# Kernel optimization log

Measured on AMD Instinct MI355X. Metric: run time of the kernel, lower is better.

Reference implementation:

```python
import jax, jax.numpy as jnp
import numpy as np

V, E, H, K, B, T = 50000, 256, 512, 12, 32, 256
START, STOP = 10, 11
NEG = -10000.0
Hd = H // 2


def _lstm(x, h0, c0, Wih, Whh, bih, bhh):
    # x: [T, B, D] -> hidden states [T, B, Hd]; PyTorch gate order i,f,g,o
    def step(carry, xt):
        h, c = carry
        g = xt @ Wih.T + bih + h @ Whh.T + bhh
        i, f, gg, o = jnp.split(g, 4, axis=-1)
        c = jax.nn.sigmoid(f) * c + jax.nn.sigmoid(i) * jnp.tanh(gg)
        h = jax.nn.sigmoid(o) * jnp.tanh(c)
        return (h, c), h
    _, hs = jax.lax.scan(step, (h0, c0), x)
    return hs


def setup_inputs() -> dict:
    key = jax.random.key(0)
    ks = jax.random.split(key, 12)
    inp = {}
    inp["sentence"] = jax.random.randint(ks[0], (B, T), 0, V, dtype=jnp.int32)
    lens = jax.random.randint(ks[1], (B,), 1, T + 1, dtype=jnp.int32)
    inp["seq_lens"] = jnp.sort(lens)[::-1]  # pack_padded requires descending
    emb = jax.random.normal(ks[2], (V, E)) * 0.05
    inp["emb"] = emb.at[0].set(0.0)  # padding_idx=0
    def lw(k):
        a, b, c, d = jax.random.split(k, 4)
        return (jax.random.normal(a, (4 * Hd, E)) * 0.05,
                jax.random.normal(b, (4 * Hd, Hd)) * 0.05,
                jax.random.normal(c, (4 * Hd,)) * 0.05,
                jax.random.normal(d, (4 * Hd,)) * 0.05)
    inp["Wih_f"], inp["Whh_f"], inp["bih_f"], inp["bhh_f"] = lw(ks[3])
    inp["Wih_b"], inp["Whh_b"], inp["bih_b"], inp["bhh_b"] = lw(ks[4])
    inp["h0"] = jax.random.normal(ks[5], (2, B, Hd))  # init_hidden uses randn
    inp["c0"] = jax.random.normal(ks[6], (2, B, Hd))
    inp["W_out"] = jax.random.normal(ks[7], (K, H)) * 0.05
    inp["b_out"] = jax.random.normal(ks[8], (K,)) * 0.05
    trans = jax.random.normal(ks[9], (K, K))
    inp["transitions"] = trans.at[START, :].set(NEG).at[:, STOP].set(NEG)
    return inp


def _features(sentence, seq_lens, emb, Wih_f, Whh_f, bih_f, bhh_f,
              Wih_b, Whh_b, bih_b, bhh_b, h0, c0, W_out, b_out):
    x = emb[sentence]                       # [B,T,E]
    t_idx = jnp.arange(T)
    # forward direction
    hf = _lstm(x.transpose(1, 0, 2), h0[0], c0[0], Wih_f, Whh_f, bih_f, bhh_f)
    hf = hf.transpose(1, 0, 2)              # [B,T,Hd]
    # backward direction: reverse each sequence within its length (packed semantics)
    rev_idx = jnp.where(t_idx[None, :] < seq_lens[:, None],
                        seq_lens[:, None] - 1 - t_idx[None, :], t_idx[None, :])  # [B,T]
    x_rev = jnp.take_along_axis(x, rev_idx[:, :, None], axis=1)
    hb_rev = _lstm(x_rev.transpose(1, 0, 2), h0[1], c0[1], Wih_b, Whh_b, bih_b, bhh_b)
    hb = jnp.take_along_axis(hb_rev.transpose(1, 0, 2), rev_idx[:, :, None], axis=1)
    hcat = jnp.concatenate([hf, hb], axis=-1)  # [B,T,H]
    return hcat @ W_out.T + b_out              # [B,T,K]


def _viterbi(feats, seq_lens, transitions):
    t_idx = jnp.arange(T)
    mask = t_idx[None, :] < seq_lens[:, None]           # [B,T]
    init = jnp.full((B, K), NEG).at[:, START].set(0.0)  # forward_var

    def vstep(fv, inputs):
        feat_t, m_t = inputs                            # [B,K], [B]
        scores = fv[:, None, :] + transitions[None, :, :]   # [B, next, prev]
        bp = jnp.argmax(scores, axis=-1)                # [B,K]
        best = jnp.max(scores, axis=-1) + feat_t
        return jnp.where(m_t[:, None], best, fv), bp

    fv, bps = jax.lax.scan(vstep, init, (feats.transpose(1, 0, 2), mask.T))
    terminal = fv + transitions[STOP][None, :]          # [B,K]
    best_last = jnp.argmax(terminal, axis=-1)           # [B]
    path_scores = jnp.take_along_axis(terminal, best_last[:, None], axis=1)[:, 0]

    def btstep(tag, inputs):
        bp_t, m_t = inputs
        pred_t = jnp.where(m_t, tag, -1)
        prev = jnp.take_along_axis(bp_t, tag[:, None], axis=1)[:, 0]
        return jnp.where(m_t, prev, tag), pred_t

    _, preds_rev = jax.lax.scan(btstep, best_last, (bps[::-1], mask.T[::-1]))
    preds = preds_rev[::-1].transpose(1, 0)             # [B,T], -1 past seq_len
    return path_scores, preds


def reference(sentence, seq_lens, emb, Wih_f, Whh_f, bih_f, bhh_f,
              Wih_b, Whh_b, bih_b, bhh_b, h0, c0, W_out, b_out, transitions):
    feats = _features(sentence, seq_lens, emb, Wih_f, Whh_f, bih_f, bhh_f,
                      Wih_b, Whh_b, bih_b, bhh_b, h0, c0, W_out, b_out)
    scores, preds = _viterbi(feats, seq_lens, transitions)
    return scores, preds
```

## Files before the change

kernel.cpp:

```cpp
#include <hip/hip_runtime.h>
#include <math.h>

#define T_ 256
#define B_ 32
#define E_ 256
#define HD_ 256
#define NG_ 1024
#define K_ 12
#define START_ 10
#define STOP_ 11
#define NEG_ -10000.0f
#define MAGICU 0x40000000u

typedef float f4_t __attribute__((ext_vector_type(4)));

__device__ __forceinline__ float sigf(float x) { return 1.0f / (1.0f + expf(-x)); }

__global__ void tok_gather(const int* __restrict__ sent, const int* __restrict__ lens,
                           int* __restrict__ tokA) {
    int e = blockIdx.x * 256 + threadIdx.x;
    int dir = e >> 13, m = e & 8191, t = m >> 5, b = m & 31;
    int len = lens[b];
    int tt = dir ? (t < len ? len - 1 - t : t) : t;
    tokA[e] = sent[b * T_ + tt];
}

__global__ void whh_tr(const float* __restrict__ Wf, const float* __restrict__ Wb,
                       float* __restrict__ WT) {
    int dir = blockIdx.x >> 8, k = blockIdx.x & 255, u = threadIdx.x;
    const float* W = dir ? Wb : Wf;
    float4 v;
    v.x = W[(0 * HD_ + u) * HD_ + k];
    v.y = W[(1 * HD_ + u) * HD_ + k];
    v.z = W[(2 * HD_ + u) * HD_ + k];
    v.w = W[(3 * HD_ + u) * HD_ + k];
    ((float4*)(WT + ((size_t)dir * 256 + k) * NG_))[u] = v;
}

__global__ void hex_init(float* __restrict__ hex) {
    int i = blockIdx.x * 256 + threadIdx.x;
    float4 m = make_float4(2.0f, 2.0f, 2.0f, 2.0f);
    ((float4*)hex)[i] = m;
}

__global__ __launch_bounds__(256) void in_gemm(
    const float* __restrict__ emb, const int* __restrict__ tokA,
    const float* __restrict__ Wih_f, const float* __restrict__ Wih_b,
    const float* __restrict__ bih_f, const float* __restrict__ bhh_f,
    const float* __restrict__ bih_b, const float* __restrict__ bhh_b,
    float* __restrict__ G) {
    const int dir = blockIdx.z;
    const int n0 = blockIdx.x * 128, m0 = blockIdx.y * 128;
    const float* Wih = dir ? Wih_b : Wih_f;
    const float* bihp = dir ? bih_b : bih_f;
    const float* bhhp = dir ? bhh_b : bhh_f;
    __shared__ float As[8][128];
    __shared__ float Bs[8][128];
    const int tid = threadIdx.x;
    const int rs = tid >> 1, kc = (tid & 1) * 4;
    const int tok = tokA[dir * 8192 + m0 + rs];
    const float* arow = emb + (size_t)tok * E_;
    const int np = n0 + rs;
    const int wrow = ((np & 3) << 8) | (np >> 2);
    const float* brow = Wih + (size_t)wrow * E_;
    const int ty = tid >> 4, tx = tid & 15;

    float acc[8][8];
#pragma unroll
    for (int i = 0; i < 8; ++i)
#pragma unroll
        for (int j = 0; j < 8; ++j) acc[i][j] = 0.f;

    for (int k0 = 0; k0 < E_; k0 += 8) {
        float4 av = *(const float4*)(arow + k0 + kc);
        float4 bv = *(const float4*)(brow + k0 + kc);
        __syncthreads();
        As[kc + 0][rs] = av.x; As[kc + 1][rs] = av.y; As[kc + 2][rs] = av.z; As[kc + 3][rs] = av.w;
        Bs[kc + 0][rs] = bv.x; Bs[kc + 1][rs] = bv.y; Bs[kc + 2][rs] = bv.z; Bs[kc + 3][rs] = bv.w;
        __syncthreads();
#pragma unroll
        for (int k = 0; k < 8; ++k) {
            float4 a0 = *(const float4*)&As[k][ty * 8];
            float4 a1 = *(const float4*)&As[k][ty * 8 + 4];
            float4 b0 = *(const float4*)&Bs[k][tx * 8];
            float4 b1 = *(const float4*)&Bs[k][tx * 8 + 4];
            float af8[8] = {a0.x, a0.y, a0.z, a0.w, a1.x, a1.y, a1.z, a1.w};
            float bf8[8] = {b0.x, b0.y, b0.z, b0.w, b1.x, b1.y, b1.z, b1.w};
#pragma unroll
            for (int i = 0; i < 8; ++i)
#pragma unroll
                for (int j = 0; j < 8; ++j) acc[i][j] += af8[i] * bf8[j];
        }
    }
    float bias[8];
#pragma unroll
    for (int j = 0; j < 8; ++j) {
        int nn = n0 + tx * 8 + j;
        int wr = ((nn & 3) << 8) | (nn >> 2);
        bias[j] = bihp[wr] + bhhp[wr];
    }
#pragma unroll
    for (int i = 0; i < 8; ++i) {
        int m = m0 + ty * 8 + i;
        float* gp = G + ((size_t)dir * 8192 + m) * NG_ + n0 + tx * 8;
        float4 o0 = {acc[i][0] + bias[0], acc[i][1] + bias[1], acc[i][2] + bias[2], acc[i][3] + bias[3]};
        float4 o1 = {acc[i][4] + bias[4], acc[i][5] + bias[5], acc[i][6] + bias[6], acc[i][7] + bias[7]};
        *(float4*)gp = o0;
        *(float4*)(gp + 4) = o1;
    }
}

__global__ __launch_bounds__(512, 1) void lstm_rec8(
    const float* __restrict__ WhhT, const float* __restrict__ G,
    const float* __restrict__ h0, const float* __restrict__ c0,
    const int* __restrict__ lens, float* __restrict__ hex) {
    const int wg = blockIdx.x;
    const int dir = wg >> 5, bt = (wg >> 3) & 3, ut = wg & 7;
    const int tid = threadIdx.x;
    const int wv = tid >> 6, ln = tid & 63;
    const int upair = ln & 15;
    const int kssub = ln >> 4;
    const int ksup = wv >> 1, bh = wv & 1;
    const int ks = ksup * 4 + kssub;
    const int sb = bh * 4 + (ln & 3);
    const int sk = ksup * 64 + (ln >> 2) * 4;
    const int speer = sk >> 5;

    __shared__ float4 hsA4[256];
    __shared__ float4 hsB4[256];
    __shared__ float4 red4[512 * 11];
    __shared__ float4 hT4[64];

    const int Tmax = lens[bt * 8];

    const float4* WT4 = (const float4*)(WhhT + (size_t)dir * 256 * NG_);
    const int gu_e = ut * 32 + upair * 2;
    float4 We[16], Wo[16];
#pragma unroll
    for (int j = 0; j < 16; ++j) {
        We[j] = WT4[(ks * 16 + j) * 256 + gu_e];
        Wo[j] = WT4[(ks * 16 + j) * 256 + gu_e + 1];
    }

    const bool is_act = (ln < 32);
    float c = 0.f;
    float4 gpend = make_float4(0.f, 0.f, 0.f, 0.f);
    const float* Gd = G + (size_t)dir * 8192 * NG_;
    if (is_act) {
        c = c0[(dir * B_ + bt * 8 + wv) * HD_ + ut * 32 + ln];
        gpend = ((const float4*)(Gd + (size_t)(bt * 8 + wv) * NG_))[ut * 32 + ln];
    }

    float* hexg = hex + (size_t)(dir * 4 + bt) * T_ * 2048;
    float4* hsX4 = bh ? hsB4 : hsA4;
    float* hsX = (float*)hsX4;

    f4_t pend;

    for (int t = 0; t < Tmax; ++t) {
        float4 hv;
        if (t == 0) {
            hv = *(const float4*)(h0 + (size_t)(dir * B_ + bt * 8 + sb) * HD_ + sk);
        } else if (speer == ut) {
            hv = hT4[sb * 8 + ((sk & 31) >> 2)];
        } else {
            asm volatile("s_waitcnt vmcnt(0)" ::: "memory");
            hv.x = pend.x; hv.y = pend.y; hv.z = pend.z; hv.w = pend.w;
            if (__float_as_uint(hv.x) == MAGICU || __float_as_uint(hv.y) == MAGICU ||
                __float_as_uint(hv.z) == MAGICU || __float_as_uint(hv.w) == MAGICU) {
                const float* src = hexg + (size_t)(t - 1) * 2048 + sb * 256 + sk;
                int it = 0;
                for (;;) {
                    __builtin_amdgcn_s_sleep(1);
                    float a0 = __hip_atomic_load(src + 0, __ATOMIC_RELAXED, __HIP_MEMORY_SCOPE_AGENT);
                    float a1 = __hip_atomic_load(src + 1, __ATOMIC_RELAXED, __HIP_MEMORY_SCOPE_AGENT);
                    float a2 = __hip_atomic_load(src + 2, __ATOMIC_RELAXED, __HIP_MEMORY_SCOPE_AGENT);
                    float a3 = __hip_atomic_load(src + 3, __ATOMIC_RELAXED, __HIP_MEMORY_SCOPE_AGENT);
                    if (!(__float_as_uint(a0) == MAGICU || __float_as_uint(a1) == MAGICU ||
                          __float_as_uint(a2) == MAGICU || __float_as_uint(a3) == MAGICU)) {
                        hv = make_float4(a0, a1, a2, a3); break;
                    }
                    if (++it > (1 << 22)) break;
                }
            }
        }
        hsX[(sk + 0) * 4 + (ln & 3)] = hv.x;
        hsX[(sk + 1) * 4 + (ln & 3)] = hv.y;
        hsX[(sk + 2) * 4 + (ln & 3)] = hv.z;
        hsX[(sk + 3) * 4 + (ln & 3)] = hv.w;
        asm volatile("s_waitcnt lgkmcnt(0)" ::: "memory");

        float4 ae0 = {0,0,0,0}, ae1 = {0,0,0,0}, ae2 = {0,0,0,0}, ae3 = {0,0,0,0};
        float4 ao0 = {0,0,0,0}, ao1 = {0,0,0,0}, ao2 = {0,0,0,0}, ao3 = {0,0,0,0};
#pragma unroll
        for (int j = 0; j < 16; ++j) {
            float4 h4 = hsX4[ks * 16 + j];
            float4 we = We[j], wo = Wo[j];
            ae0.x += we.x*h4.x; ae0.y += we.y*h4.x; ae0.z += we.z*h4.x; ae0.w += we.w*h4.x;
            ae1.x += we.x*h4.y; ae1.y += we.y*h4.y; ae1.z += we.z*h4.y; ae1.w += we.w*h4.y;
            ae2.x += we.x*h4.z; ae2.y += we.y*h4.z; ae2.z += we.z*h4.z; ae2.w += we.w*h4.z;
            ae3.x += we.x*h4.w; ae3.y += we.y*h4.w; ae3.z += we.z*h4.w; ae3.w += we.w*h4.w;
            ao0.x += wo.x*h4.x; ao0.y += wo.y*h4.x; ao0.z += wo.z*h4.x; ao0.w += wo.w*h4.x;
            ao1.x += wo.x*h4.y; ao1.y += wo.y*h4.y; ao1.z += wo.z*h4.y; ao1.w += wo.w*h4.y;
            ao2.x += wo.x*h4.z; ao2.y += wo.y*h4.z; ao2.z += wo.z*h4.z; ao2.w += wo.w*h4.z;
            ao3.x += wo.x*h4.w; ao3.y += wo.y*h4.w; ao3.z += wo.z*h4.w; ao3.w += wo.w*h4.w;
        }
        {
            float4* r = &red4[((wv * 4 + kssub) * 16 + upair) * 11 + kssub];
            r[0] = ae0; r[1] = ae1; r[2] = ae2; r[3] = ae3;
            r[4] = ao0; r[5] = ao1; r[6] = ao2; r[7] = ao3;
        }
        asm volatile("s_waitcnt lgkmcnt(0)\n\ts_barrier" ::: "memory");

        if (is_act) {
            const int b = wv, u = ln;
            const int bhv = b >> 2, bq = b & 3, up = u >> 1, par = u & 1;
            float si = gpend.x, sf = gpend.y, sg = gpend.z, so = gpend.w;
#pragma unroll
            for (int kq = 0; kq < 4; ++kq)
#pragma unroll
                for (int kr = 0; kr < 4; ++kr) {
                    float4 p = red4[(((kq * 2 + bhv) * 4 + kr) * 16 + up) * 11 + kr + par * 4 + bq];
                    si += p.x; sf += p.y; sg += p.z; so += p.w;
                }
            c = sigf(sf) * c + sigf(si) * tanhf(sg);
            float h = sigf(so) * tanhf(c);
            ((float*)hT4)[b * 32 + u] = h;
            float* dst = hexg + (size_t)t * 2048 + b * 256 + ut * 32 + u;
            asm volatile("global_store_dword %0, %1, off sc0 sc1" :: "v"(dst), "v"(h) : "memory");
            if (t + 1 < Tmax)
                gpend = ((const float4*)(Gd + ((size_t)(t + 1) * B_ + bt * 8 + b) * NG_))[ut * 32 + u];
        }
        if (t + 1 < Tmax && speer != ut) {
            const float* nsrc = hexg + (size_t)t * 2048 + sb * 256 + sk;
            asm volatile("global_load_dwordx4 %0, %1, off sc0 sc1"
                         : "=v"(pend) : "v"(nsrc) : "memory");
        }
        asm volatile("s_waitcnt lgkmcnt(0)\n\ts_barrier" ::: "memory");
    }
}

__global__ void feat_k(const float* __restrict__ hex, const int* __restrict__ lens,
                       const float* __restrict__ Wout, const float* __restrict__ bout,
                       float* __restrict__ feats) {
    int tid = threadIdx.x;
    int pl = tid / 12, k = tid % 12;
    int p = blockIdx.x * 16 + pl;
    int b = p >> 8, t = p & 255;
    int len = lens[b];
    int tr = t < len ? len - 1 - t : t;
    const float4* hf = (const float4*)(hex + ((size_t)(b >> 3) * T_ + t) * 2048 + (b & 7) * 256);
    const float4* hb = (const float4*)(hex + ((size_t)(4 + (b >> 3)) * T_ + tr) * 2048 + (b & 7) * 256);
    const float4* w0 = (const float4*)(Wout + (size_t)k * 512);
    const float4* w1 = (const float4*)(Wout + (size_t)k * 512 + 256);
    float acc = bout[k];
#pragma unroll 4
    for (int j = 0; j < 64; ++j) {
        float4 h4 = hf[j], v4 = w0[j];
        acc += h4.x * v4.x + h4.y * v4.y + h4.z * v4.z + h4.w * v4.w;
    }
#pragma unroll 4
    for (int j = 0; j < 64; ++j) {
        float4 h4 = hb[j], v4 = w1[j];
        acc += h4.x * v4.x + h4.y * v4.y + h4.z * v4.z + h4.w * v4.w;
    }
    feats[(size_t)p * K_ + k] = acc;
}

__global__ __launch_bounds__(512) void viterbi_k(
    const float* __restrict__ feats, const float* __restrict__ trans,
    const int* __restrict__ lens, float* __restrict__ out) {
    __shared__ float fv[2][B_][16];
    __shared__ float tl[K_][16];
    __shared__ unsigned char bp[T_][B_][6];
    __shared__ int best_last[B_];
    int tid = threadIdx.x;
    int b = tid >> 4, lane = tid & 15;
    if (tid < K_ * K_) tl[tid / 12][tid % 12] = trans[tid];
    if (lane < K_) fv[0][b][lane] = (lane == START_) ? 0.f : NEG_;
    __syncthreads();
    int len = lens[b];
    int pp = 0;
    float f_cur = 0.f;
    if (lane < K_) f_cur = feats[(size_t)b * T_ * K_ + lane];
    for (int t = 0; t < T_; ++t) {
        float f_nxt = 0.f;
        if (t + 1 < T_ && lane < K_) f_nxt = feats[((size_t)b * T_ + t + 1) * K_ + lane];
        if (lane < K_) {
            float best = fv[pp][b][0] + tl[lane][0];
            int argp = 0;
#pragma unroll
            for (int p = 1; p < K_; ++p) {
                float v = fv[pp][b][p] + tl[lane][p];
                if (v > best) { best = v; argp = p; }
            }
            float nb = best + f_cur;
            fv[pp ^ 1][b][lane] = (t < len) ? nb : fv[pp][b][lane];
            int other = __shfl_xor(argp, 1);
            if ((lane & 1) == 0) bp[t][b][lane >> 1] = (unsigned char)(argp | (other << 4));
        }
        __syncthreads();
        pp ^= 1;
        f_cur = f_nxt;
    }
    if (lane == 0) {
        float best = fv[pp][b][0] + tl[STOP_][0];
        int bl = 0;
#pragma unroll
        for (int p = 1; p < K_; ++p) {
            float v = fv[pp][b][p] + tl[STOP_][p];
            if (v > best) { best = v; bl = p; }
        }
        out[b] = best;
        best_last[b] = bl;
    }
    __syncthreads();
    if (lane == 0) {
        int tag = best_last[b];
        for (int t = T_ - 1; t >= 0; --t) {
            int m = (t < len);
            out[B_ + b * T_ + t] = (float)(m ? tag : -1);
            if (m) tag = (bp[t][b][tag >> 1] >> ((tag & 1) * 4)) & 15;
        }
    }
}

extern "C" void kernel_launch(void* const* d_in, const int* in_sizes, int n_in,
                              void* d_out, int out_size, void* d_ws, size_t ws_size,
                              hipStream_t stream) {
    const int*   sent  = (const int*)d_in[0];
    const int*   lens  = (const int*)d_in[1];
    const float* emb   = (const float*)d_in[2];
    const float* Wih_f = (const float*)d_in[3];
    const float* Whh_f = (const float*)d_in[4];
    const float* bih_f = (const float*)d_in[5];
    const float* bhh_f = (const float*)d_in[6];
    const float* Wih_b = (const float*)d_in[7];
    const float* Whh_b = (const float*)d_in[8];
    const float* bih_b = (const float*)d_in[9];
    const float* bhh_b = (const float*)d_in[10];
    const float* h0    = (const float*)d_in[11];
    const float* c0    = (const float*)d_in[12];
    const float* Wout  = (const float*)d_in[13];
    const float* bout  = (const float*)d_in[14];
    const float* trans = (const float*)d_in[15];
    float* out = (float*)d_out;

    char* ws = (char*)d_ws;
    int*   tokA  = (int*)ws;
    float* WhhT  = (float*)(ws + 65536);
    float* G     = (float*)(ws + 2162688);
    float* feats = (float*)(ws + 69271552);
    float* hex   = (float*)(ws + 69664768);

    tok_gather<<<64, 256, 0, stream>>>(sent, lens, tokA);
    whh_tr<<<512, 256, 0, stream>>>(Whh_f, Whh_b, WhhT);
    hex_init<<<4096, 256, 0, stream>>>(hex);
    in_gemm<<<dim3(8, 64, 2), 256, 0, stream>>>(emb, tokA, Wih_f, Wih_b,
                                                bih_f, bhh_f, bih_b, bhh_b, G);
    lstm_rec8<<<64, 512, 0, stream>>>(WhhT, G, h0, c0, lens, hex);
    feat_k<<<512, 192, 0, stream>>>(hex, lens, Wout, bout, feats);
    viterbi_k<<<1, 512, 0, stream>>>(feats, trans, lens, out);
}
```

Before: 1.130 ms.

## Split LSTM recurrence across 256 workgroups with fewer units each and swizzled LDS

The persistent recurrent kernel now uses 32 unit tiles of 8 hidden units per direction and batch tile, so the grid grows from 64 to 256 workgroups. Each workgroup holds fewer Whh weights in registers, and each thread does half as much per-step FMA work. The h staging buffer in LDS gets an XOR swizzle to reduce bank conflicts, and the reduction layout is simplified. In exchange, each step needs more cross-workgroup hidden-state traffic through global-memory polling, and only 8 lanes per wave run the activation, which could make per-step latency worse.

New measurement: 1.213 ms. +7.3%, slower.

```diff
diff --git a/kernel.cpp b/kernel.cpp
--- a/kernel.cpp
+++ b/kernel.cpp
@@ -11,6 +11,7 @@
 #define STOP_ 11
 #define NEG_ -10000.0f
 #define MAGICU 0x40000000u
+#define HSW(r) ((r) ^ (((r) >> 3) & 7))
 
 typedef float f4_t __attribute__((ext_vector_type(4)));
 
@@ -110,45 +111,42 @@
     }
 }
 
-__global__ __launch_bounds__(512, 1) void lstm_rec8(
+__global__ __launch_bounds__(512, 1) void lstm_rec16(
     const float* __restrict__ WhhT, const float* __restrict__ G,
     const float* __restrict__ h0, const float* __restrict__ c0,
     const int* __restrict__ lens, float* __restrict__ hex) {
     const int wg = blockIdx.x;
-    const int dir = wg >> 5, bt = (wg >> 3) & 3, ut = wg & 7;
+    const int dir = wg >> 7, bt = (wg >> 5) & 3, ut = wg & 31;
     const int tid = threadIdx.x;
     const int wv = tid >> 6, ln = tid & 63;
-    const int upair = ln & 15;
-    const int kssub = ln >> 4;
-    const int ksup = wv >> 1, bh = wv & 1;
-    const int ks = ksup * 4 + kssub;
+    const int bh = wv >> 2;
+    const int kq = wv & 3;
+    const int u  = ln & 7;
+    const int ks8 = kq * 8 + (ln >> 3);
     const int sb = bh * 4 + (ln & 3);
-    const int sk = ksup * 64 + (ln >> 2) * 4;
-    const int speer = sk >> 5;
+    const int sk = kq * 64 + (ln >> 2) * 4;
+    const int speer = sk >> 3;
 
     __shared__ float4 hsA4[256];
     __shared__ float4 hsB4[256];
-    __shared__ float4 red4[512 * 11];
-    __shared__ float4 hT4[64];
+    __shared__ float4 red4[512 * 10];
+    __shared__ float4 hT4[16];
 
     const int Tmax = lens[bt * 8];
 
     const float4* WT4 = (const float4*)(WhhT + (size_t)dir * 256 * NG_);
-    const int gu_e = ut * 32 + upair * 2;
-    float4 We[16], Wo[16];
-#pragma unroll
-    for (int j = 0; j < 16; ++j) {
-        We[j] = WT4[(ks * 16 + j) * 256 + gu_e];
-        Wo[j] = WT4[(ks * 16 + j) * 256 + gu_e + 1];
-    }
-
-    const bool is_act = (ln < 32);
+    const int gu = ut * 8 + u;
+    float4 Wr[8];
+#pragma unroll
+    for (int j = 0; j < 8; ++j) Wr[j] = WT4[(ks8 * 8 + j) * 256 + gu];
+
+    const bool is_act = (ln < 8);
     float c = 0.f;
     float4 gpend = make_float4(0.f, 0.f, 0.f, 0.f);
     const float* Gd = G + (size_t)dir * 8192 * NG_;
     if (is_act) {
-        c = c0[(dir * B_ + bt * 8 + wv) * HD_ + ut * 32 + ln];
-        gpend = ((const float4*)(Gd + (size_t)(bt * 8 + wv) * NG_))[ut * 32 + ln];
+        c = c0[(dir * B_ + bt * 8 + wv) * HD_ + gu];
+        gpend = ((const float4*)(Gd + (size_t)(bt * 8 + wv) * NG_))[gu];
     }
 
     float* hexg = hex + (size_t)(dir * 4 + bt) * T_ * 2048;
@@ -162,7 +160,7 @@
         if (t == 0) {
             hv = *(const float4*)(h0 + (size_t)(dir * B_ + bt * 8 + sb) * HD_ + sk);
         } else if (speer == ut) {
-            hv = hT4[sb * 8 + ((sk & 31) >> 2)];
+            hv = hT4[sb * 2 + ((sk & 7) >> 2)];
         } else {
             asm volatile("s_waitcnt vmcnt(0)" ::: "memory");
             hv.x = pend.x; hv.y = pend.y; hv.z = pend.z; hv.w = pend.w;
@@ -184,52 +182,46 @@
                 }
             }
         }
-        hsX[(sk + 0) * 4 + (ln & 3)] = hv.x;
-        hsX[(sk + 1) * 4 + (ln & 3)] = hv.y;
-        hsX[(sk + 2) * 4 + (ln & 3)] = hv.z;
-        hsX[(sk + 3) * 4 + (ln & 3)] = hv.w;
+        hsX[HSW(sk + 0) * 4 + (ln & 3)] = hv.x;
+        hsX[HSW(sk + 1) * 4 + (ln & 3)] = hv.y;
+        hsX[HSW(sk + 2) * 4 + (ln & 3)] = hv.z;
+        hsX[HSW(sk + 3) * 4 + (ln & 3)] = hv.w;
         asm volatile("s_waitcnt lgkmcnt(0)" ::: "memory");
 
-        float4 ae0 = {0,0,0,0}, ae1 = {0,0,0,0}, ae2 = {0,0,0,0}, ae3 = {0,0,0,0};
-        float4 ao0 = {0,0,0,0}, ao1 = {0,0,0,0}, ao2 = {0,0,0,0}, ao3 = {0,0,0,0};
-#pragma unroll
-        for (int j = 0; j < 16; ++j) {
-            float4 h4 = hsX4[ks * 16 + j];
-            float4 we = We[j], wo = Wo[j];
-            ae0.x += we.x*h4.x; ae0.y += we.y*h4.x; ae0.z += we.z*h4.x; ae0.w += we.w*h4.x;
-            ae1.x += we.x*h4.y; ae1.y += we.y*h4.y; ae1.z += we.z*h4.y; ae1.w += we.w*h4.y;
-            ae2.x += we.x*h4.z; ae2.y += we.y*h4.z; ae2.z += we.z*h4.z; ae2.w += we.w*h4.z;
-            ae3.x += we.x*h4.w; ae3.y += we.y*h4.w; ae3.z += we.z*h4.w; ae3.w += we.w*h4.w;
-            ao0.x += wo.x*h4.x; ao0.y += wo.y*h4.x; ao0.z += wo.z*h4.x; ao0.w += wo.w*h4.x;
-            ao1.x += wo.x*h4.y; ao1.y += wo.y*h4.y; ao1.z += wo.z*h4.y; ao1.w += wo.w*h4.y;
-            ao2.x += wo.x*h4.z; ao2.y += wo.y*h4.z; ao2.z += wo.z*h4.z; ao2.w += wo.w*h4.z;
-            ao3.x += wo.x*h4.w; ao3.y += wo.y*h4.w; ao3.z += wo.z*h4.w; ao3.w += wo.w*h4.w;
+        float4 a0 = {0,0,0,0}, a1 = {0,0,0,0}, a2 = {0,0,0,0}, a3 = {0,0,0,0};
+#pragma unroll
+        for (int j = 0; j < 8; ++j) {
+            float4 h4 = hsX4[HSW(ks8 * 8 + j)];
+            float4 w4 = Wr[j];
+            a0.x += w4.x*h4.x; a0.y += w4.y*h4.x; a0.z += w4.z*h4.x; a0.w += w4.w*h4.x;
+            a1.x += w4.x*h4.y; a1.y += w4.y*h4.y; a1.z += w4.z*h4.y; a1.w += w4.w*h4.y;
+            a2.x += w4.x*h4.z; a2.y += w4.y*h4.z; a2.z += w4.z*h4.z; a2.w += w4.w*h4.z;
+            a3.x += w4.x*h4.w; a3.y += w4.y*h4.w; a3.z += w4.z*h4.w; a3.w += w4.w*h4.w;
         }
         {
-            float4* r = &red4[((wv * 4 + kssub) * 16 + upair) * 11 + kssub];
-            r[0] = ae0; r[1] = ae1; r[2] = ae2; r[3] = ae3;
-            r[4] = ao0; r[5] = ao1; r[6] = ao2; r[7] = ao3;
+            float4* r = &red4[tid * 10];
+            r[0] = a0; r[1] = a1; r[2] = a2; r[3] = a3;
         }
         asm volatile("s_waitcnt lgkmcnt(0)\n\ts_barrier" ::: "memory");
 
         if (is_act) {
-            const int b = wv, u = ln;
-            const int bhv = b >> 2, bq = b & 3, up = u >> 1, par = u & 1;
+            const int b = wv, bq = b & 3, bh2 = b >> 2;
             float si = gpend.x, sf = gpend.y, sg = gpend.z, so = gpend.w;
 #pragma unroll
-            for (int kq = 0; kq < 4; ++kq)
-#pragma unroll
-                for (int kr = 0; kr < 4; ++kr) {
-                    float4 p = red4[(((kq * 2 + bhv) * 4 + kr) * 16 + up) * 11 + kr + par * 4 + bq];
+            for (int kq2 = 0; kq2 < 4; ++kq2)
+#pragma unroll
+                for (int ks2 = 0; ks2 < 8; ++ks2) {
+                    int tid2 = ((bh2 * 4 + kq2) * 8 + ks2) * 8 + ln;
+                    float4 p = red4[tid2 * 10 + bq];
                     si += p.x; sf += p.y; sg += p.z; so += p.w;
                 }
             c = sigf(sf) * c + sigf(si) * tanhf(sg);
             float h = sigf(so) * tanhf(c);
-            ((float*)hT4)[b * 32 + u] = h;
-            float* dst = hexg + (size_t)t * 2048 + b * 256 + ut * 32 + u;
+            ((float*)hT4)[b * 8 + ln] = h;
+            float* dst = hexg + (size_t)t * 2048 + b * 256 + gu;
             asm volatile("global_store_dword %0, %1, off sc0 sc1" :: "v"(dst), "v"(h) : "memory");
             if (t + 1 < Tmax)
-                gpend = ((const float4*)(Gd + ((size_t)(t + 1) * B_ + bt * 8 + b) * NG_))[ut * 32 + u];
+                gpend = ((const float4*)(Gd + ((size_t)(t + 1) * B_ + bt * 8 + b) * NG_))[gu];
         }
         if (t + 1 < Tmax && speer != ut) {
             const float* nsrc = hexg + (size_t)t * 2048 + sb * 256 + sk;
@@ -358,7 +350,7 @@
     hex_init<<<4096, 256, 0, stream>>>(hex);
     in_gemm<<<dim3(8, 64, 2), 256, 0, stream>>>(emb, tokA, Wih_f, Wih_b,
                                                 bih_f, bhh_f, bih_b, bhh_b, G);
-    lstm_rec8<<<64, 512, 0, stream>>>(WhhT, G, h0, c0, lens, hex);
+    lstm_rec16<<<256, 512, 0, stream>>>(WhhT, G, h0, c0, lens, hex);
     feat_k<<<512, 192, 0, stream>>>(hex, lens, Wout, bout, feats);
     viterbi_k<<<1, 512, 0, stream>>>(feats, trans, lens, out);
 }
```

## Fuse input GEMM with LSTM recurrence in one persistent launch using per-tile readiness flags

Applied to the files above, without the earlier changes.

Merges three prep kernels into one launch. Fuses the input-projection GEMM and the recurrent LSTM into a single kernel: 64 blocks run the recurrence while the other blocks compute GEMM tiles and bump per-row-block atomic counters. The recurrence waits on those counters, so the time loop can start before the whole gate precompute is done. This overlaps GEMM with recurrence and removes launch gaps. In exchange it adds spin-wait polling, smaller GEMM tiles per thread, and relies on the recurrence blocks being co-resident with GEMM blocks.

New measurement: 1.112 ms. About the same (-1.6%).

```diff
diff --git a/kernel.cpp b/kernel.cpp
--- a/kernel.cpp
+++ b/kernel.cpp
@@ -16,107 +16,128 @@
 
 __device__ __forceinline__ float sigf(float x) { return 1.0f / (1.0f + expf(-x)); }
 
-__global__ void tok_gather(const int* __restrict__ sent, const int* __restrict__ lens,
-                           int* __restrict__ tokA) {
-    int e = blockIdx.x * 256 + threadIdx.x;
-    int dir = e >> 13, m = e & 8191, t = m >> 5, b = m & 31;
-    int len = lens[b];
-    int tt = dir ? (t < len ? len - 1 - t : t) : t;
-    tokA[e] = sent[b * T_ + tt];
+__global__ void prep(const int* __restrict__ sent, const int* __restrict__ lens,
+                     int* __restrict__ tokA, const float* __restrict__ Wf,
+                     const float* __restrict__ Wb, float* __restrict__ WT,
+                     float* __restrict__ hex, int* __restrict__ gcnt) {
+    const int b = blockIdx.x, tid = threadIdx.x;
+    if (b < 4096) {
+        float4 m = make_float4(2.0f, 2.0f, 2.0f, 2.0f);
+        ((float4*)hex)[b * 256 + tid] = m;
+    } else if (b < 4608) {
+        int b2 = b - 4096;
+        int dir = b2 >> 8, k = b2 & 255, u = tid;
+        const float* W = dir ? Wb : Wf;
+        float4 v;
+        v.x = W[(0 * HD_ + u) * HD_ + k];
+        v.y = W[(1 * HD_ + u) * HD_ + k];
+        v.z = W[(2 * HD_ + u) * HD_ + k];
+        v.w = W[(3 * HD_ + u) * HD_ + k];
+        ((float4*)(WT + ((size_t)dir * 256 + k) * NG_))[u] = v;
+    } else {
+        int e = (b - 4608) * 256 + tid;
+        if (e < 128) gcnt[e] = 0;
+        int dir = e >> 13, m = e & 8191, t = m >> 5, bb = m & 31;
+        int len = lens[bb];
+        int tt = dir ? (t < len ? len - 1 - t : t) : t;
+        tokA[e] = sent[bb * T_ + tt];
+    }
 }
 
-__global__ void whh_tr(const float* __restrict__ Wf, const float* __restrict__ Wb,
-                       float* __restrict__ WT) {
-    int dir = blockIdx.x >> 8, k = blockIdx.x & 255, u = threadIdx.x;
-    const float* W = dir ? Wb : Wf;
-    float4 v;
-    v.x = W[(0 * HD_ + u) * HD_ + k];
-    v.y = W[(1 * HD_ + u) * HD_ + k];
-    v.z = W[(2 * HD_ + u) * HD_ + k];
-    v.w = W[(3 * HD_ + u) * HD_ + k];
-    ((float4*)(WT + ((size_t)dir * 256 + k) * NG_))[u] = v;
-}
-
-__global__ void hex_init(float* __restrict__ hex) {
-    int i = blockIdx.x * 256 + threadIdx.x;
-    float4 m = make_float4(2.0f, 2.0f, 2.0f, 2.0f);
-    ((float4*)hex)[i] = m;
-}
-
-__global__ __launch_bounds__(256) void in_gemm(
+__global__ __launch_bounds__(512, 1) void mega(
     const float* __restrict__ emb, const int* __restrict__ tokA,
     const float* __restrict__ Wih_f, const float* __restrict__ Wih_b,
     const float* __restrict__ bih_f, const float* __restrict__ bhh_f,
     const float* __restrict__ bih_b, const float* __restrict__ bhh_b,
-    float* __restrict__ G) {
-    const int dir = blockIdx.z;
-    const int n0 = blockIdx.x * 128, m0 = blockIdx.y * 128;
-    const float* Wih = dir ? Wih_b : Wih_f;
-    const float* bihp = dir ? bih_b : bih_f;
-    const float* bhhp = dir ? bhh_b : bhh_f;
-    __shared__ float As[8][128];
-    __shared__ float Bs[8][128];
+    const float* __restrict__ WhhT, float* __restrict__ G,
+    const float* __restrict__ h0, const float* __restrict__ c0,
+    const int* __restrict__ lens, float* __restrict__ hex,
+    int* __restrict__ gcnt) {
+    __shared__ float smem[24832];
     const int tid = threadIdx.x;
-    const int rs = tid >> 1, kc = (tid & 1) * 4;
-    const int tok = tokA[dir * 8192 + m0 + rs];
-    const float* arow = emb + (size_t)tok * E_;
-    const int np = n0 + rs;
-    const int wrow = ((np & 3) << 8) | (np >> 2);
-    const float* brow = Wih + (size_t)wrow * E_;
-    const int ty = tid >> 4, tx = tid & 15;
-
-    float acc[8][8];
-#pragma unroll
-    for (int i = 0; i < 8; ++i)
-#pragma unroll
-        for (int j = 0; j < 8; ++j) acc[i][j] = 0.f;
-
-    for (int k0 = 0; k0 < E_; k0 += 8) {
-        float4 av = *(const float4*)(arow + k0 + kc);
-        float4 bv = *(const float4*)(brow + k0 + kc);
+
+    if (blockIdx.x >= 64) {
+        const int bi = blockIdx.x - 64;
+        const int by = bi >> 4, sub = bi & 15;
+        const int dir = sub >> 3, bx = sub & 7;
+        const int n0 = bx * 128, m0 = by * 128;
+        float* As = smem;
+        float* Bs = smem + 1024;
+        const int rs = (tid & 255) >> 1, kc = (tid & 1) * 4;
+        const float* srow;
+        if (tid < 256) {
+            int tok = tokA[dir * 8192 + m0 + rs];
+            srow = emb + (size_t)tok * E_;
+        } else {
+            int np = n0 + rs;
+            int wrow = ((np & 3) << 8) | (np >> 2);
+            srow = (dir ? Wih_b : Wih_f) + (size_t)wrow * E_;
+        }
+        float* Ls = (tid < 256) ? As : Bs;
+        const int ty = tid >> 4, tx = tid & 15;
+
+        float acc[4][8];
+#pragma unroll
+        for (int i = 0; i < 4; ++i)
+#pragma unroll
+            for (int j = 0; j < 8; ++j) acc[i][j] = 0.f;
+
+        for (int k0 = 0; k0 < E_; k0 += 8) {
+            float4 v = *(const float4*)(srow + k0 + kc);
+            __syncthreads();
+            Ls[(kc + 0) * 128 + rs] = v.x;
+            Ls[(kc + 1) * 128 + rs] = v.y;
+            Ls[(kc + 2) * 128 + rs] = v.z;
+            Ls[(kc + 3) * 128 + rs] = v.w;
+            __syncthreads();
+#pragma unroll
+            for (int k = 0; k < 8; ++k) {
+                float4 a  = *(const float4*)&As[k * 128 + ty * 4];
+                float4 b0 = *(const float4*)&Bs[k * 128 + tx * 8];
+                float4 b1 = *(const float4*)&Bs[k * 128 + tx * 8 + 4];
+                float af[4] = {a.x, a.y, a.z, a.w};
+                float bf[8] = {b0.x, b0.y, b0.z, b0.w, b1.x, b1.y, b1.z, b1.w};
+#pragma unroll
+                for (int i = 0; i < 4; ++i)
+#pragma unroll
+                    for (int j = 0; j < 8; ++j) acc[i][j] += af[i] * bf[j];
+            }
+        }
+        const float* bihp = dir ? bih_b : bih_f;
+        const float* bhhp = dir ? bhh_b : bhh_f;
+        float bias[8];
+#pragma unroll
+        for (int j = 0; j < 8; ++j) {
+            int nn = n0 + tx * 8 + j;
+            int wr = ((nn & 3) << 8) | (nn >> 2);
+            bias[j] = bihp[wr] + bhhp[wr];
+        }
+#pragma unroll
+        for (int i = 0; i < 4; ++i) {
+            int m = m0 + ty * 4 + i;
+            float* gp = G + ((size_t)dir * 8192 + m) * NG_ + n0 + tx * 8;
+            f4_t o0, o1;
+            o0.x = acc[i][0] + bias[0]; o0.y = acc[i][1] + bias[1];
+            o0.z = acc[i][2] + bias[2]; o0.w = acc[i][3] + bias[3];
+            o1.x = acc[i][4] + bias[4]; o1.y = acc[i][5] + bias[5];
+            o1.z = acc[i][6] + bias[6]; o1.w = acc[i][7] + bias[7];
+            asm volatile("global_store_dwordx4 %0, %1, off sc0 sc1" :: "v"(gp), "v"(o0) : "memory");
+            asm volatile("global_store_dwordx4 %0, %1, off sc0 sc1" :: "v"(gp + 4), "v"(o1) : "memory");
+        }
+        asm volatile("s_waitcnt vmcnt(0)" ::: "memory");
         __syncthreads();
-        As[kc + 0][rs] = av.x; As[kc + 1][rs] = av.y; As[kc + 2][rs] = av.z; As[kc + 3][rs] = av.w;
-        Bs[kc + 0][rs] = bv.x; Bs[kc + 1][rs] = bv.y; Bs[kc + 2][rs] = bv.z; Bs[kc + 3][rs] = bv.w;
-        __syncthreads();
-#pragma unroll
-        for (int k = 0; k < 8; ++k) {
-            float4 a0 = *(const float4*)&As[k][ty * 8];
-            float4 a1 = *(const float4*)&As[k][ty * 8 + 4];
-            float4 b0 = *(const float4*)&Bs[k][tx * 8];
-            float4 b1 = *(const float4*)&Bs[k][tx * 8 + 4];
-            float af8[8] = {a0.x, a0.y, a0.z, a0.w, a1.x, a1.y, a1.z, a1.w};
-            float bf8[8] = {b0.x, b0.y, b0.z, b0.w, b1.x, b1.y, b1.z, b1.w};
-#pragma unroll
-            for (int i = 0; i < 8; ++i)
-#pragma unroll
-                for (int j = 0; j < 8; ++j) acc[i][j] += af8[i] * bf8[j];
-        }
-    }
-    float bias[8];
-#pragma unroll
-    for (int j = 0; j < 8; ++j) {
-        int nn = n0 + tx * 8 + j;
-        int wr = ((nn & 3) << 8) | (nn >> 2);
-        bias[j] = bihp[wr] + bhhp[wr];
-    }
-#pragma unroll
-    for (int i = 0; i < 8; ++i) {
-        int m = m0 + ty * 8 + i;
-        float* gp = G + ((size_t)dir * 8192 + m) * NG_ + n0 + tx * 8;
-        float4 o0 = {acc[i][0] + bias[0], acc[i][1] + bias[1], acc[i][2] + bias[2], acc[i][3] + bias[3]};
-        float4 o1 = {acc[i][4] + bias[4], acc[i][5] + bias[5], acc[i][6] + bias[6], acc[i][7] + bias[7]};
-        *(float4*)gp = o0;
-        *(float4*)(gp + 4) = o1;
-    }
-}
-
-__global__ __launch_bounds__(512, 1) void lstm_rec8(
-    const float* __restrict__ WhhT, const float* __restrict__ G,
-    const float* __restrict__ h0, const float* __restrict__ c0,
-    const int* __restrict__ lens, float* __restrict__ hex) {
+        if (tid == 0)
+            __hip_atomic_fetch_add(gcnt + dir * 64 + by, 1, __ATOMIC_RELEASE, __HIP_MEMORY_SCOPE_AGENT);
+        return;
+    }
+
+    float4* red4 = (float4*)smem;
+    float4* hsA4 = (float4*)(smem + 22528);
+    float4* hsB4 = (float4*)(smem + 23552);
+    float4* hT4  = (float4*)(smem + 24576);
+
     const int wg = blockIdx.x;
     const int dir = wg >> 5, bt = (wg >> 3) & 3, ut = wg & 7;
-    const int tid = threadIdx.x;
     const int wv = tid >> 6, ln = tid & 63;
     const int upair = ln & 15;
     const int kssub = ln >> 4;
@@ -126,11 +147,6 @@
     const int sk = ksup * 64 + (ln >> 2) * 4;
     const int speer = sk >> 5;
 
-    __shared__ float4 hsA4[256];
-    __shared__ float4 hsB4[256];
-    __shared__ float4 red4[512 * 11];
-    __shared__ float4 hT4[64];
-
     const int Tmax = lens[bt * 8];
 
     const float4* WT4 = (const float4*)(WhhT + (size_t)dir * 256 * NG_);
@@ -140,12 +156,21 @@
     for (int j = 0; j < 16; ++j) {
         We[j] = WT4[(ks * 16 + j) * 256 + gu_e];
         Wo[j] = WT4[(ks * 16 + j) * 256 + gu_e + 1];
+    }
+
+    {
+        int it = 0;
+        while (__hip_atomic_load(gcnt + dir * 64, __ATOMIC_RELAXED, __HIP_MEMORY_SCOPE_AGENT) < 8) {
+            __builtin_amdgcn_s_sleep(8);
+            if (++it > (1 << 22)) break;
+        }
     }
 
     const bool is_act = (ln < 32);
     float c = 0.f;
     float4 gpend = make_float4(0.f, 0.f, 0.f, 0.f);
     const float* Gd = G + (size_t)dir * 8192 * NG_;
+    int gok = 1, gready = 0;
     if (is_act) {
         c = c0[(dir * B_ + bt * 8 + wv) * HD_ + ut * 32 + ln];
         gpend = ((const float4*)(Gd + (size_t)(bt * 8 + wv) * NG_))[ut * 32 + ln];
@@ -215,6 +240,20 @@
         if (is_act) {
             const int b = wv, u = ln;
             const int bhv = b >> 2, bq = b & 3, up = u >> 1, par = u & 1;
+            if (!gok) {
+                const int byc = t >> 2;
+                int itc = 0;
+                while (__hip_atomic_load(gcnt + dir * 64 + byc, __ATOMIC_RELAXED,
+                                         __HIP_MEMORY_SCOPE_AGENT) < 8) {
+                    __builtin_amdgcn_s_sleep(2);
+                    if (++itc > (1 << 22)) break;
+                }
+                const float* gsrc = Gd + ((size_t)t * B_ + bt * 8 + b) * NG_ + (size_t)(ut * 32 + u) * 4;
+                f4_t tmp;
+                asm volatile("global_load_dwordx4 %0, %1, off sc0 sc1\n\ts_waitcnt vmcnt(0)"
+                             : "=v"(tmp) : "v"(gsrc) : "memory");
+                gpend = make_float4(tmp.x, tmp.y, tmp.z, tmp.w);
+            }
             float si = gpend.x, sf = gpend.y, sg = gpend.z, so = gpend.w;
 #pragma unroll
             for (int kq = 0; kq < 4; ++kq)
@@ -228,8 +267,20 @@
             ((float*)hT4)[b * 32 + u] = h;
             float* dst = hexg + (size_t)t * 2048 + b * 256 + ut * 32 + u;
             asm volatile("global_store_dword %0, %1, off sc0 sc1" :: "v"(dst), "v"(h) : "memory");
-            if (t + 1 < Tmax)
-                gpend = ((const float4*)(Gd + ((size_t)(t + 1) * B_ + bt * 8 + b) * NG_))[ut * 32 + u];
+            if (t + 1 < Tmax) {
+                const int byn = (t + 1) >> 2;
+                if (byn > gready) {
+                    int la = byn + 7; if (la > 63) la = 63;
+                    if (__hip_atomic_load(gcnt + dir * 64 + la, __ATOMIC_RELAXED,
+                                          __HIP_MEMORY_SCOPE_AGENT) >= 8) gready = la;
+                    else if (__hip_atomic_load(gcnt + dir * 64 + byn, __ATOMIC_RELAXED,
+                                               __HIP_MEMORY_SCOPE_AGENT) >= 8) gready = byn;
+                }
+                if (byn <= gready) {
+                    gpend = ((const float4*)(Gd + ((size_t)(t + 1) * B_ + bt * 8 + b) * NG_))[ut * 32 + u];
+                    gok = 1;
+                } else gok = 0;
+            }
         }
         if (t + 1 < Tmax && speer != ut) {
             const float* nsrc = hexg + (size_t)t * 2048 + sb * 256 + sk;
@@ -352,13 +403,11 @@
     float* G     = (float*)(ws + 2162688);
     float* feats = (float*)(ws + 69271552);
     float* hex   = (float*)(ws + 69664768);
-
-    tok_gather<<<64, 256, 0, stream>>>(sent, lens, tokA);
-    whh_tr<<<512, 256, 0, stream>>>(Whh_f, Whh_b, WhhT);
-    hex_init<<<4096, 256, 0, stream>>>(hex);
-    in_gemm<<<dim3(8, 64, 2), 256, 0, stream>>>(emb, tokA, Wih_f, Wih_b,
-                                                bih_f, bhh_f, bih_b, bhh_b, G);
-    lstm_rec8<<<64, 512, 0, stream>>>(WhhT, G, h0, c0, lens, hex);
+    int*   gcnt  = (int*)feats;
+
+    prep<<<4672, 256, 0, stream>>>(sent, lens, tokA, Whh_f, Whh_b, WhhT, hex, gcnt);
+    mega<<<1088, 512, 0, stream>>>(emb, tokA, Wih_f, Wih_b, bih_f, bhh_f, bih_b, bhh_b,
+                                   WhhT, G, h0, c0, lens, hex, gcnt);
     feat_k<<<512, 192, 0, stream>>>(hex, lens, Wout, bout, feats);
     viterbi_k<<<1, 512, 0, stream>>>(feats, trans, lens, out);
 }
```
